# Performance work log

Hardware: AMD Instinct MI355X
Metric: run time of the kernel (lower is better)

Reference implementation:

```python
import jax, jax.numpy as jnp
import numpy as np

L = 2048  # sequence length
V = 2048  # num_tokens == channel width (one-hot embedding)
B = 4     # batch


def _pos_bias(v_table):
    # pos[i,j] = max(i-j, 0); embed via [L,1] table -> [L,L]
    i = jnp.arange(L)
    pos = jnp.maximum(i[:, None] - i[None, :], 0)
    return v_table[pos, 0]


def setup_inputs() -> dict:
    key = jax.random.key(0)
    ks = jax.random.split(key, 11)
    idx = jax.random.randint(ks[0], (B, L), 0, V)
    lin = lambda k, std: (jax.random.normal(k, (V, V), dtype=jnp.float32) * std)
    return {
        "idx": idx,
        # layer_zero: all std=1 (explicit re-init in torch code)
        "Wq0": lin(ks[1], 1.0), "Wk0": lin(ks[2], 1.0), "Wv0": lin(ks[3], 1.0),
        # layer_one: Wk std=1 (re-init), Wv std=0.02 (default init); Wq is zero-fn
        "Wk1": lin(ks[4], 1.0), "Wv1": lin(ks[5], 0.02),
        # layer_two: Wq,Wv std=1 (re-init), Wk std=0.02 (default)
        "Wq2": lin(ks[6], 1.0), "Wk2": lin(ks[7], 0.02), "Wv2": lin(ks[8], 1.0),
        # relative-position embedding tables [L,1], std=0.02
        "v0": jax.random.normal(ks[9], (L, 1), dtype=jnp.float32) * 0.02,
        "v1": jax.random.normal(ks[10], (L, 1), dtype=jnp.float32) * 0.02,
    }


def reference(idx, Wq0, Wk0, Wv0, Wk1, Wv1, Wq2, Wk2, Wv2, v0, v1):
    e = jax.nn.one_hot(idx, V, dtype=jnp.float32)            # [B,L,V]
    tril = jnp.tril(jnp.ones((L, L), dtype=bool))
    p0 = _pos_bias(v0)                                       # [L,L]
    p1 = _pos_bias(v1)

    # layer_zero(e, e): scores = Q@K^T + sum_e(K)[:,None]*pos, tril, @V (no softmax)
    K0 = e @ Wk0.T
    Q0 = e @ Wq0.T
    V0 = e @ Wv0.T
    s0 = jnp.einsum('bqv,bkv->bqk', Q0, K0) + K0.sum(-1)[:, :, None] * p0[None]
    l0 = jnp.where(tril, s0, 0.0) @ V0                       # [B,L,V]

    # layer_one(l0, e): Wq is zero-fn -> only the pos-bias term survives
    K1 = e @ Wk1.T
    V1 = l0 @ Wv1.T
    s1 = K1.sum(-1)[:, :, None] * p1[None]
    l1 = jnp.where(tril, s1, 0.0) @ V1

    # layer_two(e, l1): v is zero-fn -> no pos bias
    K2 = l1 @ Wk2.T
    Q2 = e @ Wq2.T
    V2 = e @ Wv2.T
    s2 = jnp.einsum('bqv,bkv->bqk', Q2, K2)
    logits = jnp.where(tril, s2, 0.0) @ V2                   # [B,L,V]
    return logits
```

## Files before the change

### kernel.cpp

```cpp
#include <hip/hip_runtime.h>

typedef float f32x4 __attribute__((ext_vector_type(4)));
typedef short s16x8 __attribute__((ext_vector_type(8)));

constexpr int L = 2048;
constexpr int V = 2048;
constexpr int NB = 4;
constexpr size_t VV  = (size_t)V * V;
constexpr size_t BLV = (size_t)NB * L * V;
constexpr size_t LV  = (size_t)L * V;

__device__ __forceinline__ unsigned short f2bf(float f) {
    unsigned u = __float_as_uint(f);
    u = (u + 0x7FFFu + ((u >> 16) & 1u)) >> 16;
    return (unsigned short)u;
}
__device__ __forceinline__ float bf2f(unsigned short s) {
    return __uint_as_float(((unsigned)s) << 16);
}

__device__ __forceinline__ void gload16(const unsigned short* g, unsigned short* l) {
    auto gp = (const __attribute__((address_space(1))) unsigned int*)g;
    auto lp = (__attribute__((address_space(3))) unsigned int*)l;
    __builtin_amdgcn_global_load_lds(gp, lp, 16, 0, 0);
}


__device__ __forceinline__ void stage2(const unsigned short* A, const unsigned short* B,
                                       int m0, int n0, int k0, unsigned short* buf,
                                       int wave, int lane) {
    int rl = lane >> 2, csl = lane & 3;
    #pragma unroll
    for (int h = 0; h < 2; ++h) {
        int rr = wave * 32 + h * 16;
        int row = rr + rl;
        int ch = csl ^ ((row >> 1) & 3);
        size_t ga = (size_t)row * 2048 + k0 + ch * 8;
        gload16(A + (size_t)m0 * 2048 + ga, buf + rr * 32);
        gload16(B + (size_t)n0 * 2048 + ga, buf + 8192 + rr * 32);
    }
}

__device__ __forceinline__ s16x8 frag(const unsigned short* arr, int row, int kc) {
    int cs = kc ^ ((row >> 1) & 3);
    return *(const s16x8*)&arr[row * 32 + cs * 8];
}

struct KLoopOut { f32x4 acc[8][4]; };

__device__ __forceinline__ void kloop(const unsigned short* Ab, const unsigned short* Bb,
                                      int m0, int n0, int NKB, unsigned short* lds,
                                      int wave, int lane, int wr, int wc,
                                      f32x4 (&acc)[8][4]) {
    const int r15 = lane & 15, kc = lane >> 4;

    stage2(Ab, Bb, m0, n0, 0,  lds,         wave, lane);
    stage2(Ab, Bb, m0, n0, 32, lds + 16384, wave, lane);
    stage2(Ab, Bb, m0, n0, 64, lds + 32768, wave, lane);
    asm volatile("s_waitcnt vmcnt(8)" ::: "memory");
    __builtin_amdgcn_sched_barrier(0);
    __builtin_amdgcn_s_barrier();
    __builtin_amdgcn_sched_barrier(0);

    for (int t = 0; t < NKB; ++t) {
        const unsigned short* cur = lds + (t & 3) * 16384;
        unsigned short* nxt = lds + ((t + 3) & 3) * 16384;
        const int rem = NKB - 1 - t;

        s16x8 bfr[4], afr[4];
        #pragma unroll
        for (int nf = 0; nf < 4; ++nf)
            bfr[nf] = frag(cur + 8192, wc * 64 + nf * 16 + r15, kc);
        #pragma unroll
        for (int mf = 0; mf < 4; ++mf)
            afr[mf] = frag(cur, wr * 128 + mf * 16 + r15, kc);
        if (rem >= 3)
            stage2(Ab, Bb, m0, n0, (t + 3) * 32, nxt, wave, lane);
        __builtin_amdgcn_sched_barrier(0);
        __builtin_amdgcn_s_barrier();
        __builtin_amdgcn_sched_barrier(0);
        __builtin_amdgcn_s_setprio(1);
        #pragma unroll
        for (int mf = 0; mf < 4; ++mf)
            #pragma unroll
            for (int nf = 0; nf < 4; ++nf)
                acc[mf][nf] = __builtin_amdgcn_mfma_f32_16x16x32_bf16(afr[mf], bfr[nf], acc[mf][nf], 0, 0, 0);
        __builtin_amdgcn_s_setprio(0);
        __builtin_amdgcn_sched_barrier(0);
        __builtin_amdgcn_s_barrier();
        __builtin_amdgcn_sched_barrier(0);

        s16x8 afr2[4];
        #pragma unroll
        for (int mf = 0; mf < 4; ++mf)
            afr2[mf] = frag(cur, wr * 128 + (mf + 4) * 16 + r15, kc);
        __builtin_amdgcn_sched_barrier(0);
        __builtin_amdgcn_s_barrier();
        __builtin_amdgcn_sched_barrier(0);
        __builtin_amdgcn_s_setprio(1);
        #pragma unroll
        for (int mf = 0; mf < 4; ++mf)
            #pragma unroll
            for (int nf = 0; nf < 4; ++nf)
                acc[mf + 4][nf] = __builtin_amdgcn_mfma_f32_16x16x32_bf16(afr2[mf], bfr[nf], acc[mf + 4][nf], 0, 0, 0);
        __builtin_amdgcn_s_setprio(0);
        __builtin_amdgcn_sched_barrier(0);
        if (rem >= 3)      { asm volatile("s_waitcnt vmcnt(8)" ::: "memory"); }
        else if (rem == 2) { asm volatile("s_waitcnt vmcnt(4)" ::: "memory"); }
        else if (rem == 1) { asm volatile("s_waitcnt vmcnt(0)" ::: "memory"); }
        __builtin_amdgcn_s_barrier();
        __builtin_amdgcn_sched_barrier(0);
    }
}

template<int OUTM, bool TOEP>
__global__ __launch_bounds__(512, 2) void gemm_big(
    const unsigned short* __restrict__ A, size_t sA,
    const unsigned short* __restrict__ B, size_t sB,
    float* __restrict__ outF, unsigned short* __restrict__ outH, size_t sO,
    const int* __restrict__ idxp, const float* __restrict__ ks)
{
    __shared__ __align__(16) unsigned short lds[4 * 16384];

    const int tid  = threadIdx.x;
    const int lane = tid & 63, wave = tid >> 6;
    const int wr = wave >> 2, wc = wave & 3;
    const int bz = blockIdx.z;
    int bx = blockIdx.x, by = blockIdx.y;
    if constexpr (TOEP) { int tswap = bx; bx = by; by = tswap; }
    const int m0 = by * 256, n0 = bx * 256;
    const int r15 = lane & 15, kc = lane >> 4;

    const unsigned short* Ab = A + (size_t)bz * sA;
    const unsigned short* Bb = B + (size_t)bz * sB;
    const int NKB = TOEP ? 8 * (bx + 1) : 64;

    f32x4 acc[8][4];
    const f32x4 zf = {0.f, 0.f, 0.f, 0.f};
    #pragma unroll
    for (int i = 0; i < 8; ++i)
        #pragma unroll
        for (int j = 0; j < 4; ++j) acc[i][j] = zf;

    kloop(Ab, Bb, m0, n0, NKB, lds, wave, lane, wr, wc, acc);

    float csc[4];
    if constexpr (TOEP) {
        #pragma unroll
        for (int nf = 0; nf < 4; ++nf) {
            int gcol = n0 + wc * 64 + nf * 16 + r15;
            csc[nf] = ks[idxp[bz * L + gcol]];
        }
    }
    #pragma unroll
    for (int mf = 0; mf < 8; ++mf) {
        #pragma unroll
        for (int r = 0; r < 4; ++r) {
            int grow = m0 + wr * 128 + mf * 16 + kc * 4 + r;
            #pragma unroll
            for (int nf = 0; nf < 4; ++nf) {
                float v = acc[mf][nf][r];
                if constexpr (TOEP) v *= csc[nf];
                int gcol = n0 + wc * 64 + nf * 16 + r15;
                size_t o = (size_t)bz * sO + (size_t)grow * 2048 + gcol;
                if constexpr (OUTM == 0) outF[o] = v;
                else                     outH[o] = f2bf(v);
            }
        }
    }
}

struct PDesc { const unsigned short* A; const unsigned short* B; float* oF; unsigned short* oH; };

__global__ __launch_bounds__(512, 2) void gemm_pre_big(PDesc d0, PDesc d1, PDesc d2) {
    PDesc d = (blockIdx.z == 0) ? d0 : (blockIdx.z == 1) ? d1 : d2;
    __shared__ __align__(16) unsigned short lds[4 * 16384];

    const int tid  = threadIdx.x;
    const int lane = tid & 63, wave = tid >> 6;
    const int wr = wave >> 2, wc = wave & 3;
    const int m0 = blockIdx.y * 256, n0 = blockIdx.x * 256;
    const int r15 = lane & 15, kc = lane >> 4;

    f32x4 acc[8][4];
    const f32x4 zf = {0.f, 0.f, 0.f, 0.f};
    #pragma unroll
    for (int i = 0; i < 8; ++i)
        #pragma unroll
        for (int j = 0; j < 4; ++j) acc[i][j] = zf;

    kloop(d.A, d.B, m0, n0, 64, lds, wave, lane, wr, wc, acc);

    const bool isF = (d.oF != nullptr);
    #pragma unroll
    for (int mf = 0; mf < 8; ++mf) {
        #pragma unroll
        for (int r = 0; r < 4; ++r) {
            int grow = m0 + wr * 128 + mf * 16 + kc * 4 + r;
            #pragma unroll
            for (int nf = 0; nf < 4; ++nf) {
                float v = acc[mf][nf][r];
                int gcol = n0 + wc * 64 + nf * 16 + r15;
                size_t o = (size_t)grow * 2048 + gcol;
                if (isF) d.oF[o] = v;
                else     d.oH[o] = f2bf(v);
            }
        }
    }
}


__global__ __launch_bounds__(256) void colsum_atomic(const float* __restrict__ W,
                                                     float* __restrict__ out) {
    int r0 = blockIdx.x * 8;
    int c = threadIdx.x;
    float s[8];
    #pragma unroll
    for (int i = 0; i < 8; ++i) s[i] = 0.f;
    for (int r = 0; r < 8; ++r) {
        const float* row = W + (size_t)(r0 + r) * V;
        #pragma unroll
        for (int i = 0; i < 8; ++i) s[i] += row[c + i * 256];
    }
    #pragma unroll
    for (int i = 0; i < 8; ++i) atomicAdd(&out[c + i * 256], s[i]);
}

__global__ void init_kernel(float* __restrict__ ks0, float* __restrict__ ks1) {
    int i = blockIdx.x * 256 + threadIdx.x;
    if (i < 2048) { ks0[i] = 0.f; ks1[i] = 0.f; }
}

__global__ __launch_bounds__(256) void tb_fill(const float* __restrict__ v1,
                                               unsigned short* __restrict__ TBh) {
    int n = blockIdx.x;
    int c0 = threadIdx.x * 8;
    s16x8 hv;
    #pragma unroll
    for (int i = 0; i < 8; ++i) {
        int k = c0 + i;
        float f = (k <= n) ? v1[n - k] : 0.f;
        hv[i] = (short)f2bf(f);
    }
    *(s16x8*)&TBh[(size_t)n * 2048 + c0] = hv;
}

struct TDesc { const float* A; unsigned short* Th; };

__global__ void transpose_cast_multi(TDesc d0, TDesc d1, TDesc d2, TDesc d3, TDesc d4) {
    TDesc d;
    switch (blockIdx.z) {
        case 0: d = d0; break;
        case 1: d = d1; break;
        case 2: d = d2; break;
        case 3: d = d3; break;
        default: d = d4; break;
    }
    __shared__ float tile[32][33];
    int x = blockIdx.x * 32 + threadIdx.x;
    int y0 = blockIdx.y * 32;
    for (int r = threadIdx.y; r < 32; r += 8)
        tile[r][threadIdx.x] = d.A[(size_t)(y0 + r) * V + x];
    __syncthreads();
    int xo = blockIdx.y * 32 + threadIdx.x;
    int yo0 = blockIdx.x * 32;
    for (int r = threadIdx.y; r < 32; r += 8)
        d.Th[(size_t)(yo0 + r) * V + xo] = f2bf(tile[threadIdx.x][r]);
}

__global__ __launch_bounds__(256) void cast_kernel(const float* __restrict__ A,
                                                   unsigned short* __restrict__ H,
                                                   int n4) {
    int i = blockIdx.x * 256 + threadIdx.x;
    if (i >= n4) return;
    float4 f = ((const float4*)A)[i];
    ushort4 h;
    h.x = f2bf(f.x); h.y = f2bf(f.y); h.z = f2bf(f.z); h.w = f2bf(f.w);
    ((ushort4*)H)[i] = h;
}


__global__ __launch_bounds__(256) void scatterA_kernel(const int* __restrict__ idx,
                                                       const float* __restrict__ G0,
                                                       const float* __restrict__ ks0,
                                                       const float* __restrict__ v0,
                                                       unsigned short* __restrict__ Th) {
    __shared__ float buck[8 * 2048];
    int tid = threadIdx.x;
    const float4 z4 = make_float4(0.f, 0.f, 0.f, 0.f);
    for (int i = tid; i < 8 * 2048 / 4; i += 256) ((float4*)buck)[i] = z4;
    __syncthreads();

    int b = blockIdx.y, q0 = blockIdx.x * 8;
    int qr = tid >> 5, kl = tid & 31;
    int q = q0 + qr;
    int iq = idx[b * L + q];
    float kq = ks0[iq];
    const float* Grow = G0 + (size_t)iq * V;
    for (int k = kl; k <= q; k += 32) {
        int ik = idx[b * L + k];
        float val = Grow[ik] + kq * v0[q - k];
        atomicAdd(&buck[qr * 2048 + ik], val);
    }
    __syncthreads();
    size_t base = ((size_t)b * L + q0) * V;
    for (int i = tid; i < 8 * 2048; i += 256)
        Th[base + i] = f2bf(buck[i]);
}

__global__ __launch_bounds__(256) void scatterC_kernel(const int* __restrict__ idx,
                                                       const unsigned short* __restrict__ T2h,
                                                       unsigned short* __restrict__ Th) {
    __shared__ float buck[8 * 2048];
    int tid = threadIdx.x;
    const float4 z4 = make_float4(0.f, 0.f, 0.f, 0.f);
    for (int i = tid; i < 8 * 2048 / 4; i += 256) ((float4*)buck)[i] = z4;
    __syncthreads();

    int b = blockIdx.y, q0 = blockIdx.x * 8;
    int qr = tid >> 5, kl = tid & 31;
    int q = q0 + qr;
    int iq = idx[b * L + q];
    const unsigned short* Trow = T2h + ((size_t)b * V + iq) * L;
    for (int k = kl; k <= q; k += 32) {
        int ik = idx[b * L + k];
        atomicAdd(&buck[qr * 2048 + ik], bf2f(Trow[k]));
    }
    __syncthreads();
    size_t base = ((size_t)b * L + q0) * V;
    for (int i = tid; i < 8 * 2048; i += 256)
        Th[base + i] = f2bf(buck[i]);
}


extern "C" void kernel_launch(void* const* d_in, const int* in_sizes, int n_in,
                              void* d_out, int out_size, void* d_ws, size_t ws_size,
                              hipStream_t stream) {
    (void)in_sizes; (void)n_in; (void)out_size; (void)ws_size;
    const int*   idx = (const int*)d_in[0];
    const float* Wq0 = (const float*)d_in[1];
    const float* Wk0 = (const float*)d_in[2];
    const float* Wv0 = (const float*)d_in[3];
    const float* Wk1 = (const float*)d_in[4];
    const float* Wv1 = (const float*)d_in[5];
    const float* Wq2 = (const float*)d_in[6];
    const float* Wk2 = (const float*)d_in[7];
    const float* Wv2 = (const float*)d_in[8];
    const float* v0  = (const float*)d_in[9];
    const float* v1  = (const float*)d_in[10];
    float* out = (float*)d_out;

    char* W = (char*)d_ws;
    const size_t MiB = 1024 * 1024;

    unsigned short* PPT = (unsigned short*)W;
    unsigned short* TAh = (unsigned short*)W;
    unsigned short* T2h = (unsigned short*)W;
    unsigned short* Y1 = (unsigned short*)(W + 64 * MiB);
    unsigned short* Y2 = (unsigned short*)(W + 72 * MiB);
    unsigned short* Uh  = (unsigned short*)(W + 64 * MiB);
    unsigned short* TCh = Uh;
    float* Gf = (float*)(W + 96 * MiB);
    unsigned short* Y4 = (unsigned short*)(W + 112 * MiB);
    unsigned short* X1 = (unsigned short*)(W + 128 * MiB);
    unsigned short* X2 = (unsigned short*)(W + 136 * MiB);
    unsigned short* X3 = (unsigned short*)(W + 144 * MiB);
    unsigned short* X4 = (unsigned short*)(W + 152 * MiB);
    unsigned short* TBh = X3;
    float* ks0 = (float*)(W + 192 * MiB);
    float* ks1 = (float*)(W + 192 * MiB + 16 * 1024);

    dim3 blk(256);

    {
        TDesc t0{Wq0, X1}, t1{Wk0, X2}, t2{Wq2, X3}, t3{Wk2, X4}, t4{Wv0, Y1};
        transpose_cast_multi<<<dim3(64, 64, 5), dim3(32, 8), 0, stream>>>(t0, t1, t2, t3, t4);
    }
    cast_kernel<<<dim3((int)(VV / 4 / 256)), blk, 0, stream>>>(Wv1, Y2, (int)(VV / 4));
    init_kernel<<<dim3(8), blk, 0, stream>>>(ks0, ks1);
    colsum_atomic<<<dim3(256), blk, 0, stream>>>(Wk0, ks0);
    colsum_atomic<<<dim3(256), blk, 0, stream>>>(Wk1, ks1);

    {
        PDesc dG{X1, X2, Gf, nullptr};
        PDesc dM{X3, X4, nullptr, Y4};
        PDesc dP{Y1, Y2, nullptr, PPT};
        gemm_pre_big<<<dim3(8, 8, 3), dim3(512), 0, stream>>>(dG, dM, dP);
    }
    tb_fill<<<dim3(2048), blk, 0, stream>>>(v1, TBh);
    {
        PDesc dR{Y4, PPT, nullptr, X1};
        gemm_pre_big<<<dim3(8, 8, 1), dim3(512), 0, stream>>>(dR, dR, dR);
    }

    scatterA_kernel<<<dim3(L / 8, NB), blk, 0, stream>>>(idx, Gf, ks0, v0, TAh);

    gemm_big<1, false><<<dim3(8, 8, NB), dim3(512), 0, stream>>>(
        X1, 0, TAh, LV, nullptr, Uh, LV, nullptr, nullptr);

    gemm_big<1, true><<<dim3(8, 8, NB), dim3(512), 0, stream>>>(
        Uh, LV, TBh, 0, nullptr, T2h, LV, idx, ks1);

    scatterC_kernel<<<dim3(L / 8, NB), blk, 0, stream>>>(idx, T2h, TCh);

    cast_kernel<<<dim3((int)(VV / 4 / 256)), blk, 0, stream>>>(Wv2, X2, (int)(VV / 4));

    gemm_big<0, false><<<dim3(8, 32, 1), dim3(512), 0, stream>>>(
        TCh, 0, X2, 0, out, nullptr, 0, nullptr, nullptr);
}
```

Measured before the change: 536.1 us.

## Split-K the single-tile precompute GEMM and widen scatter kernels to 64-lane rows

```diff
diff --git a/kernel.cpp b/kernel.cpp
--- a/kernel.cpp
+++ b/kernel.cpp
@@ -45,8 +45,6 @@
     int cs = kc ^ ((row >> 1) & 3);
     return *(const s16x8*)&arr[row * 32 + cs * 8];
 }
-
-struct KLoopOut { f32x4 acc[8][4]; };
 
 __device__ __forceinline__ void kloop(const unsigned short* Ab, const unsigned short* Bb,
                                       int m0, int n0, int NKB, unsigned short* lds,
@@ -209,6 +207,61 @@
     }
 }
 
+__global__ __launch_bounds__(512, 2) void gemm_preK(const unsigned short* __restrict__ A,
+                                                    const unsigned short* __restrict__ B,
+                                                    float* __restrict__ outP) {
+    __shared__ __align__(16) unsigned short lds[4 * 16384];
+
+    const int tid  = threadIdx.x;
+    const int lane = tid & 63, wave = tid >> 6;
+    const int wr = wave >> 2, wc = wave & 3;
+    const int m0 = blockIdx.y * 256, n0 = blockIdx.x * 256;
+    const int r15 = lane & 15, kc = lane >> 4;
+    const int z = blockIdx.z;
+
+    const unsigned short* Ab = A + z * 512;
+    const unsigned short* Bb = B + z * 512;
+    float* outF = outP + (size_t)z * VV;
+
+    f32x4 acc[8][4];
+    const f32x4 zf = {0.f, 0.f, 0.f, 0.f};
+    #pragma unroll
+    for (int i = 0; i < 8; ++i)
+        #pragma unroll
+        for (int j = 0; j < 4; ++j) acc[i][j] = zf;
+
+    kloop(Ab, Bb, m0, n0, 16, lds, wave, lane, wr, wc, acc);
+
+    #pragma unroll
+    for (int mf = 0; mf < 8; ++mf) {
+        #pragma unroll
+        for (int r = 0; r < 4; ++r) {
+            int grow = m0 + wr * 128 + mf * 16 + kc * 4 + r;
+            #pragma unroll
+            for (int nf = 0; nf < 4; ++nf) {
+                int gcol = n0 + wc * 64 + nf * 16 + r15;
+                outF[(size_t)grow * 2048 + gcol] = acc[mf][nf][r];
+            }
+        }
+    }
+}
+
+__global__ __launch_bounds__(256) void reduce4_cast(const float* __restrict__ P,
+                                                    unsigned short* __restrict__ H) {
+    int i = blockIdx.x * 256 + threadIdx.x;
+    const float4* p0 = (const float4*)P;
+    const float4* p1 = (const float4*)(P + VV);
+    const float4* p2 = (const float4*)(P + 2 * VV);
+    const float4* p3 = (const float4*)(P + 3 * VV);
+    float4 a = p0[i], b = p1[i], c = p2[i], d = p3[i];
+    ushort4 h;
+    h.x = f2bf(a.x + b.x + c.x + d.x);
+    h.y = f2bf(a.y + b.y + c.y + d.y);
+    h.z = f2bf(a.z + b.z + c.z + d.z);
+    h.w = f2bf(a.w + b.w + c.w + d.w);
+    ((ushort4*)H)[i] = h;
+}
+
 
 __global__ __launch_bounds__(256) void colsum_atomic(const float* __restrict__ W,
                                                      float* __restrict__ out) {
@@ -285,51 +338,88 @@
                                                        const float* __restrict__ ks0,
                                                        const float* __restrict__ v0,
                                                        unsigned short* __restrict__ Th) {
-    __shared__ float buck[8 * 2048];
+    __shared__ float buck[4 * 2048];
     int tid = threadIdx.x;
     const float4 z4 = make_float4(0.f, 0.f, 0.f, 0.f);
-    for (int i = tid; i < 8 * 2048 / 4; i += 256) ((float4*)buck)[i] = z4;
+    #pragma unroll
+    for (int i = 0; i < 8; ++i) ((float4*)buck)[tid + i * 256] = z4;
     __syncthreads();
 
-    int b = blockIdx.y, q0 = blockIdx.x * 8;
-    int qr = tid >> 5, kl = tid & 31;
+    int b = blockIdx.y, q0 = blockIdx.x * 4;
+    int qr = tid >> 6, lane = tid & 63;
     int q = q0 + qr;
-    int iq = idx[b * L + q];
+    const int* idxb = idx + b * L;
+    int iq = idxb[q];
     float kq = ks0[iq];
     const float* Grow = G0 + (size_t)iq * V;
-    for (int k = kl; k <= q; k += 32) {
-        int ik = idx[b * L + k];
-        float val = Grow[ik] + kq * v0[q - k];
-        atomicAdd(&buck[qr * 2048 + ik], val);
+    float* brow = buck + qr * 2048;
+
+    int k = lane;
+    for (; k + 192 <= q; k += 256) {
+        int i0 = idxb[k], i1 = idxb[k + 64], i2 = idxb[k + 128], i3 = idxb[k + 192];
+        float g0 = Grow[i0], g1 = Grow[i1], g2 = Grow[i2], g3 = Grow[i3];
+        float w0 = v0[q - k], w1 = v0[q - k - 64], w2 = v0[q - k - 128], w3 = v0[q - k - 192];
+        atomicAdd(&brow[i0], g0 + kq * w0);
+        atomicAdd(&brow[i1], g1 + kq * w1);
+        atomicAdd(&brow[i2], g2 + kq * w2);
+        atomicAdd(&brow[i3], g3 + kq * w3);
+    }
+    for (; k <= q; k += 64) {
+        int ik = idxb[k];
+        atomicAdd(&brow[ik], Grow[ik] + kq * v0[q - k]);
     }
     __syncthreads();
     size_t base = ((size_t)b * L + q0) * V;
-    for (int i = tid; i < 8 * 2048; i += 256)
-        Th[base + i] = f2bf(buck[i]);
+    #pragma unroll
+    for (int it = 0; it < 4; ++it) {
+        int i = tid + it * 256;
+        s16x8 hv;
+        #pragma unroll
+        for (int j = 0; j < 8; ++j) hv[j] = (short)f2bf(buck[i * 8 + j]);
+        *(s16x8*)&Th[base + (size_t)i * 8] = hv;
+    }
 }
 
 __global__ __launch_bounds__(256) void scatterC_kernel(const int* __restrict__ idx,
                                                        const unsigned short* __restrict__ T2h,
                                                        unsigned short* __restrict__ Th) {
-    __shared__ float buck[8 * 2048];
+    __shared__ float buck[4 * 2048];
     int tid = threadIdx.x;
     const float4 z4 = make_float4(0.f, 0.f, 0.f, 0.f);
-    for (int i = tid; i < 8 * 2048 / 4; i += 256) ((float4*)buck)[i] = z4;
+    #pragma unroll
+    for (int i = 0; i < 8; ++i) ((float4*)buck)[tid + i * 256] = z4;
     __syncthreads();
 
-    int b = blockIdx.y, q0 = blockIdx.x * 8;
-    int qr = tid >> 5, kl = tid & 31;
+    int b = blockIdx.y, q0 = blockIdx.x * 4;
+    int qr = tid >> 6, lane = tid & 63;
     int q = q0 + qr;
-    int iq = idx[b * L + q];
+    const int* idxb = idx + b * L;
+    int iq = idxb[q];
     const unsigned short* Trow = T2h + ((size_t)b * V + iq) * L;
-    for (int k = kl; k <= q; k += 32) {
-        int ik = idx[b * L + k];
-        atomicAdd(&buck[qr * 2048 + ik], bf2f(Trow[k]));
-    }
+    float* brow = buck + qr * 2048;
+
+    int k = lane;
+    for (; k + 192 <= q; k += 256) {
+        int i0 = idxb[k], i1 = idxb[k + 64], i2 = idxb[k + 128], i3 = idxb[k + 192];
+        float t0 = bf2f(Trow[k]), t1 = bf2f(Trow[k + 64]);
+        float t2 = bf2f(Trow[k + 128]), t3 = bf2f(Trow[k + 192]);
+        atomicAdd(&brow[i0], t0);
+        atomicAdd(&brow[i1], t1);
+        atomicAdd(&brow[i2], t2);
+        atomicAdd(&brow[i3], t3);
+    }
+    for (; k <= q; k += 64)
+        atomicAdd(&brow[idxb[k]], bf2f(Trow[k]));
     __syncthreads();
     size_t base = ((size_t)b * L + q0) * V;
-    for (int i = tid; i < 8 * 2048; i += 256)
-        Th[base + i] = f2bf(buck[i]);
+    #pragma unroll
+    for (int it = 0; it < 4; ++it) {
+        int i = tid + it * 256;
+        s16x8 hv;
+        #pragma unroll
+        for (int j = 0; j < 8; ++j) hv[j] = (short)f2bf(buck[i * 8 + j]);
+        *(s16x8*)&Th[base + (size_t)i * 8] = hv;
+    }
 }
 
 
@@ -356,6 +446,7 @@
     unsigned short* PPT = (unsigned short*)W;
     unsigned short* TAh = (unsigned short*)W;
     unsigned short* T2h = (unsigned short*)W;
+    float* Rp = (float*)(W + 8 * MiB);
     unsigned short* Y1 = (unsigned short*)(W + 64 * MiB);
     unsigned short* Y2 = (unsigned short*)(W + 72 * MiB);
     unsigned short* Uh  = (unsigned short*)(W + 64 * MiB);
@@ -388,12 +479,10 @@
         gemm_pre_big<<<dim3(8, 8, 3), dim3(512), 0, stream>>>(dG, dM, dP);
     }
     tb_fill<<<dim3(2048), blk, 0, stream>>>(v1, TBh);
-    {
-        PDesc dR{Y4, PPT, nullptr, X1};
-        gemm_pre_big<<<dim3(8, 8, 1), dim3(512), 0, stream>>>(dR, dR, dR);
-    }
-
-    scatterA_kernel<<<dim3(L / 8, NB), blk, 0, stream>>>(idx, Gf, ks0, v0, TAh);
+    gemm_preK<<<dim3(8, 8, 4), dim3(512), 0, stream>>>(Y4, PPT, Rp);
+    reduce4_cast<<<dim3((int)(VV / 4 / 256)), blk, 0, stream>>>(Rp, X1);
+
+    scatterA_kernel<<<dim3(L / 4, NB), blk, 0, stream>>>(idx, Gf, ks0, v0, TAh);
 
     gemm_big<1, false><<<dim3(8, 8, NB), dim3(512), 0, stream>>>(
         X1, 0, TAh, LV, nullptr, Uh, LV, nullptr, nullptr);
@@ -401,7 +490,7 @@
     gemm_big<1, true><<<dim3(8, 8, NB), dim3(512), 0, stream>>>(
         Uh, LV, TBh, 0, nullptr, T2h, LV, idx, ks1);
 
-    scatterC_kernel<<<dim3(L / 8, NB), blk, 0, stream>>>(idx, T2h, TCh);
+    scatterC_kernel<<<dim3(L / 4, NB), blk, 0, stream>>>(idx, T2h, TCh);
 
     cast_kernel<<<dim3((int)(VV / 4 / 256)), blk, 0, stream>>>(Wv2, X2, (int)(VV / 4));
 
```

Result: faster. 491.0 us (-8.4%).
